# Optimization experiments

Measured on AMD Instinct MI355X. Metric: run time of the kernel, lower is better.

The kernel has to match this reference:

```python
import jax, jax.numpy as jnp
import numpy as np

N_AA = 300000
N_PROT = 30000
D_AA = 128
D_PROT = 128
HID = 128
OUT = 64
E_AP = 300000
E_PP = 960000
BATCH = 16384
NEG_SLOPE = 0.2


def _gatv2(x_src, x_dst, src, dst, Wl, bl, Wr, br, att, bias, num_dst):
    # GATv2Conv (heads=1): e_ij = att . leaky_relu(Wl x_j + Wr x_i); softmax over dst; out_i = sum alpha_ij * (Wl x_j) + bias
    xl = x_src @ Wl + bl                      # [Ns, C]
    xr = x_dst @ Wr + br                      # [Nd, C]
    e = jax.nn.leaky_relu(xl[src] + xr[dst], NEG_SLOPE)   # [E, C]
    logits = e @ att                          # [E]
    lmax = jax.ops.segment_max(logits, dst, num_segments=num_dst)
    ex = jnp.exp(logits - lmax[dst])
    denom = jax.ops.segment_sum(ex, dst, num_segments=num_dst)
    alpha = ex / denom[dst]                   # [E]
    msg = xl[src] * alpha[:, None]            # [E, C]
    out = jax.ops.segment_sum(msg, dst, num_segments=num_dst)
    return out + bias


def setup_inputs() -> dict:
    key = jax.random.key(0)
    ks = jax.random.split(key, 16)
    s = 0.05
    x_aa = jax.random.normal(ks[0], (N_AA, D_AA), jnp.float32)
    x_prot = jax.random.normal(ks[1], (N_PROT, D_PROT), jnp.float32)
    edge_index_ap = jnp.stack([
        jax.random.randint(ks[2], (E_AP,), 0, N_AA),
        jax.random.randint(ks[3], (E_AP,), 0, N_PROT)])
    edge_index_pp = jnp.stack([
        jax.random.randint(ks[4], (E_PP,), 0, N_PROT),
        jax.random.randint(ks[5], (E_PP,), 0, N_PROT)])
    return {
        'x_aa': x_aa, 'x_prot': x_prot,
        'edge_index_ap': edge_index_ap, 'edge_index_pp': edge_index_pp,
        'batch_size': BATCH,
        'Wl_ap': s * jax.random.normal(ks[6], (D_AA, HID), jnp.float32),
        'bl_ap': jnp.zeros((HID,), jnp.float32),
        'Wr_ap': s * jax.random.normal(ks[7], (D_PROT, HID), jnp.float32),
        'br_ap': jnp.zeros((HID,), jnp.float32),
        'att_ap': s * jax.random.normal(ks[8], (HID,), jnp.float32),
        'bias_ap': jnp.zeros((HID,), jnp.float32),
        'Wl_pp': s * jax.random.normal(ks[9], (D_PROT, HID), jnp.float32),
        'bl_pp': jnp.zeros((HID,), jnp.float32),
        'Wr_pp': s * jax.random.normal(ks[10], (D_PROT, HID), jnp.float32),
        'br_pp': jnp.zeros((HID,), jnp.float32),
        'att_pp': s * jax.random.normal(ks[11], (HID,), jnp.float32),
        'bias_pp': jnp.zeros((HID,), jnp.float32),
        'W_lin': s * jax.random.normal(ks[12], (HID, OUT), jnp.float32),
        'b_lin': jnp.zeros((OUT,), jnp.float32),
    }


def reference(x_aa, x_prot, edge_index_ap, edge_index_pp, batch_size,
              Wl_ap, bl_ap, Wr_ap, br_ap, att_ap, bias_ap,
              Wl_pp, bl_pp, Wr_pp, br_pp, att_pp, bias_pp,
              W_lin, b_lin):
    out_ap = _gatv2(x_aa, x_prot, edge_index_ap[0], edge_index_ap[1],
                    Wl_ap, bl_ap, Wr_ap, br_ap, att_ap, bias_ap, N_PROT)
    out_pp = _gatv2(x_prot, x_prot, edge_index_pp[0], edge_index_pp[1],
                    Wl_pp, bl_pp, Wr_pp, br_pp, att_pp, bias_pp, N_PROT)
    x = out_ap + out_pp                      # HeteroConv aggr='sum'
    x = jax.nn.relu(x[:batch_size])
    return x @ W_lin + b_lin
```

## Files before the change

kernel.cpp:

```cpp
#include <hip/hip_runtime.h>
#include <hip/hip_bf16.h>

typedef __attribute__((ext_vector_type(8))) short short8;
typedef __attribute__((ext_vector_type(4))) unsigned short ushort4_t;
typedef __attribute__((ext_vector_type(4))) float f32x4;

#define CAP_AP 64
#define CAP_PP 128

__device__ __forceinline__ unsigned short f2bf(float f) {
  unsigned u = __float_as_uint(f);
  u += 0x7FFFu + ((u >> 16) & 1u);
  return (unsigned short)(u >> 16);
}

__global__ __launch_bounds__(256) void k_init(
    int* __restrict__ map, int* __restrict__ cnt_ap, int* __restrict__ cnt_pp,
    int* __restrict__ ccount, int n_aa, int batch)
{
  int i = blockIdx.x * 256 + threadIdx.x;
  if (i < n_aa) map[i] = -1;
  if (i < batch) { cnt_ap[i] = 0; cnt_pp[i] = 0; }
  if (i == 0) *ccount = 0;
}

__global__ __launch_bounds__(256) void k_edges(
    const int* __restrict__ ei_ap, const int* __restrict__ ei_pp,
    int* __restrict__ map, int* __restrict__ cnt_ap, int* __restrict__ cnt_pp,
    int* __restrict__ csr_ap, int* __restrict__ csr_pp,
    int e_ap, int e_pp, int nb_ap, int batch)
{
  int b = blockIdx.x;
  if (b < nb_ap) {
    int e = b * 256 + threadIdx.x;
    if (e < e_ap) {
      int d = ei_ap[e_ap + e];
      if (d < batch) {
        int s = ei_ap[e];
        int pos = atomicAdd(&cnt_ap[d], 1);
        if (pos < CAP_AP) csr_ap[d * CAP_AP + pos] = s;
        map[s] = 1;
      }
    }
  } else {
    int e = (b - nb_ap) * 256 + threadIdx.x;
    if (e < e_pp) {
      int d = ei_pp[e_pp + e];
      if (d < batch) {
        int pos = atomicAdd(&cnt_pp[d], 1);
        if (pos < CAP_PP) csr_pp[d * CAP_PP + pos] = ei_pp[e];
      }
    }
  }
}

__global__ __launch_bounds__(256) void k_assign(
    int* __restrict__ map, int* __restrict__ inv, int* __restrict__ ccount, int n)
{
  int i = blockIdx.x * 256 + threadIdx.x;
  bool need = (i < n) && (map[i] == 1);
  unsigned long long m = __ballot(need);
  if (m == 0ull) return;
  int lane = threadIdx.x & 63;
  int pre = __popcll(m & ((1ull << lane) - 1ull));
  int leader = __ffsll((unsigned long long)m) - 1;
  int base = 0;
  if (lane == leader) base = atomicAdd(ccount, __popcll(m));
  base = __shfl(base, leader, 64);
  if (need) {
    int slot = base + pre;
    map[i] = slot;
    inv[slot] = i;
  }
}

struct GemmJob {
  const float* X; const int* inv; const int* rowsp; int M;
  const float* W; const float* bias; unsigned short* Y; int nb;
};

__device__ __forceinline__ void gemm_body(const GemmJob& J, int bid, short8* lwb)
{
  const int tid = threadIdx.x;
  const int rows = J.rowsp ? *J.rowsp : J.M;

  {
    unsigned short* lw16 = (unsigned short*)lwb;
#pragma unroll
    for (int p = 0; p < 16; ++p) {
      int fi = p * 1024 + tid * 4;
      float4 w4 = *(const float4*)(J.W + fi);
#pragma unroll
      for (int q = 0; q < 4; ++q) {
        int k = (fi + q) >> 7, n = (fi + q) & 127;
        float wv = (q == 0) ? w4.x : (q == 1) ? w4.y : (q == 2) ? w4.z : w4.w;
        lw16[(((k >> 5) * 8 + (n >> 4)) * 64 + ((k >> 3) & 3) * 16 + (n & 15)) * 8 + (k & 7)] = f2bf(wv);
      }
    }
  }

  const int wave = tid >> 6;
  const int lane = tid & 63;
  const int quad = lane >> 4;
  const int l16  = lane & 15;
  __syncthreads();

  for (int tile = bid; tile * 64 < rows; tile += J.nb) {
    int ra = tile * 64 + wave * 16 + l16;
    long xrow = -1;
    if (ra < rows) xrow = J.inv ? (long)J.inv[ra] : (long)ra;

    short8 xf[4];
#pragma unroll
    for (int kt = 0; kt < 4; ++kt) {
      short8 a = {};
      if (xrow >= 0) {
        const float* p = J.X + xrow * 128 + kt * 32 + quad * 8;
        float4 x0 = ((const float4*)p)[0];
        float4 x1 = ((const float4*)p)[1];
        a[0] = (short)f2bf(x0.x); a[1] = (short)f2bf(x0.y);
        a[2] = (short)f2bf(x0.z); a[3] = (short)f2bf(x0.w);
        a[4] = (short)f2bf(x1.x); a[5] = (short)f2bf(x1.y);
        a[6] = (short)f2bf(x1.z); a[7] = (short)f2bf(x1.w);
      }
      xf[kt] = a;
    }

    f32x4 accs[8];
#pragma unroll
    for (int nt = 0; nt < 8; ++nt) {
      f32x4 acc = {0.f, 0.f, 0.f, 0.f};
#pragma unroll
      for (int kt = 0; kt < 4; ++kt)
        acc = __builtin_amdgcn_mfma_f32_16x16x32_bf16(lwb[(kt * 8 + nt) * 64 + lane], xf[kt], acc, 0, 0, 0);
      accs[nt] = acc;
    }

    if (ra < rows) {
      unsigned short* yp = J.Y + (long)ra * 128;
#pragma unroll
      for (int nt = 0; nt < 8; ++nt) {
        int col = nt * 16 + quad * 4;
        float4 bv = *(const float4*)(J.bias + col);
        ushort4_t v;
        v[0] = f2bf(accs[nt][0] + bv.x);
        v[1] = f2bf(accs[nt][1] + bv.y);
        v[2] = f2bf(accs[nt][2] + bv.z);
        v[3] = f2bf(accs[nt][3] + bv.w);
        *(ushort4_t*)(yp + col) = v;
      }
    }
  }
}

__global__ __launch_bounds__(256) void k_mega(
    GemmJob j0, GemmJob j1, GemmJob j2, GemmJob j3,
    const int* __restrict__ map, const int* __restrict__ cnt_ap,
    int* __restrict__ csr_ap, int nb_gemm, int nb_remap, int batch)
{
  __shared__ short8 lwb[4 * 8 * 64];
  int b = blockIdx.x;
  if (b < nb_gemm) {
    if (b < j0.nb)                      gemm_body(j0, b, lwb);
    else if (b < j0.nb + j1.nb)         gemm_body(j1, b - j0.nb, lwb);
    else if (b < j0.nb + j1.nb + j2.nb) gemm_body(j2, b - j0.nb - j1.nb, lwb);
    else                                gemm_body(j3, b - j0.nb - j1.nb - j2.nb, lwb);
  } else {
    int i = (b - nb_gemm) * 256 + threadIdx.x;
    if (i < batch * CAP_AP) {
      int d = i / CAP_AP;
      int slot = i - d * CAP_AP;
      int n = cnt_ap[d]; if (n > CAP_AP) n = CAP_AP;
      if (slot < n) csr_ap[i] = map[csr_ap[i]];
    }
  }
}

__global__ __launch_bounds__(256) void k_gat_final(
    const int* __restrict__ cnt_ap, const int* __restrict__ csr_ap,
    const unsigned short* __restrict__ xl_aa,
    const unsigned short* __restrict__ xr_ap, const float* __restrict__ att_ap,
    const int* __restrict__ cnt_pp, const int* __restrict__ csr_pp,
    const unsigned short* __restrict__ xl_pp,
    const unsigned short* __restrict__ xr_pp, const float* __restrict__ att_pp,
    const float* __restrict__ bias_ap, const float* __restrict__ bias_pp,
    const float* __restrict__ W_lin, const float* __restrict__ b_lin,
    float* __restrict__ out, int batch)
{
  __shared__ unsigned lw2[64 * 64];
  __shared__ float lh[4][128];
  for (int e = threadIdx.x; e < 4096; e += 256) {
    int cp = e >> 6, o = e & 63;
    unsigned lo = f2bf(W_lin[(2 * cp) * 64 + o]);
    unsigned hi = f2bf(W_lin[(2 * cp + 1) * 64 + o]);
    lw2[e] = lo | (hi << 16);
  }

  const int wave = threadIdx.x >> 6;
  const int lane = threadIdx.x & 63;
  const int dst = blockIdx.x * 4 + wave;
  const int c0 = 2 * lane;

  float h0 = 0.f, h1 = 0.f;
  if (dst < batch) {
    h0 = bias_ap[c0] + bias_pp[c0];
    h1 = bias_ap[c0 + 1] + bias_pp[c0 + 1];

#pragma unroll
    for (int type = 0; type < 2; ++type) {
      const int* cnt  = type ? cnt_pp : cnt_ap;
      const int* csr  = type ? csr_pp : csr_ap;
      const int cap   = type ? CAP_PP : CAP_AP;
      const unsigned short* xl = type ? xl_pp : xl_aa;
      const unsigned short* xr = type ? xr_pp : xr_ap;
      const float* att = type ? att_pp : att_ap;

      int n = __builtin_amdgcn_readfirstlane(cnt[dst]);
      if (n > cap) n = cap;
      const long base = (long)dst * cap;
      unsigned upr = *(const unsigned*)(xr + (long)dst * 128 + c0);
      float xr0 = __uint_as_float(upr << 16);
      float xr1 = __uint_as_float(upr & 0xffff0000u);
      float2 at = *(const float2*)(att + c0);

      float l = 0.f, o0 = 0.f, o1 = 0.f;
      int j = 0;
      for (; j + 4 <= n; j += 4) {
        int si[4]; unsigned u[4];
#pragma unroll
        for (int q = 0; q < 4; ++q) si[q] = csr[base + j + q];
#pragma unroll
        for (int q = 0; q < 4; ++q)
          u[q] = *(const unsigned*)(xl + (long)si[q] * 128 + c0);
        float pv[4], a0v[4], a1v[4];
#pragma unroll
        for (int q = 0; q < 4; ++q) {
          float a0 = __uint_as_float(u[q] << 16);
          float a1 = __uint_as_float(u[q] & 0xffff0000u);
          a0v[q] = a0; a1v[q] = a1;
          float e0 = a0 + xr0; e0 = e0 > 0.f ? e0 : 0.2f * e0;
          float e1 = a1 + xr1; e1 = e1 > 0.f ? e1 : 0.2f * e1;
          pv[q] = at.x * e0 + at.y * e1;
        }
#pragma unroll
        for (int off = 32; off; off >>= 1) {
#pragma unroll
          for (int q = 0; q < 4; ++q) pv[q] += __shfl_xor(pv[q], off, 64);
        }
#pragma unroll
        for (int q = 0; q < 4; ++q) {
          float w = __expf(pv[q]);
          l += w;
          o0 = fmaf(w, a0v[q], o0);
          o1 = fmaf(w, a1v[q], o1);
        }
      }
      for (; j < n; ++j) {
        int sA = csr[base + j];
        unsigned uA = *(const unsigned*)(xl + (long)sA * 128 + c0);
        float a0 = __uint_as_float(uA << 16), a1 = __uint_as_float(uA & 0xffff0000u);
        float e0 = a0 + xr0; e0 = e0 > 0.f ? e0 : 0.2f * e0;
        float e1 = a1 + xr1; e1 = e1 > 0.f ? e1 : 0.2f * e1;
        float pA = at.x * e0 + at.y * e1;
#pragma unroll
        for (int off = 32; off; off >>= 1) pA += __shfl_xor(pA, off, 64);
        float w = __expf(pA);
        l += w;
        o0 = fmaf(w, a0, o0);
        o1 = fmaf(w, a1, o1);
      }
      float invl = (l > 0.f) ? 1.f / l : 0.f;
      h0 = fmaf(o0, invl, h0);
      h1 = fmaf(o1, invl, h1);
    }
  }

  lh[wave][c0]     = h0 > 0.f ? h0 : 0.f;
  lh[wave][c0 + 1] = h1 > 0.f ? h1 : 0.f;
  __syncthreads();

  if (dst < batch) {
    float acc = b_lin[lane];
#pragma unroll 16
    for (int cp = 0; cp < 64; ++cp) {
      unsigned u = lw2[cp * 64 + lane];
      acc = fmaf(lh[wave][2 * cp],     __uint_as_float(u << 16),        acc);
      acc = fmaf(lh[wave][2 * cp + 1], __uint_as_float(u & 0xffff0000u), acc);
    }
    out[(long)dst * 64 + lane] = acc;
  }
}

extern "C" void kernel_launch(void* const* d_in, const int* in_sizes, int n_in,
                              void* d_out, int out_size, void* d_ws, size_t ws_size,
                              hipStream_t stream)
{
  const float* x_aa   = (const float*)d_in[0];
  const float* x_prot = (const float*)d_in[1];
  const int*   ei_ap  = (const int*)d_in[2];
  const int*   ei_pp  = (const int*)d_in[3];
  const float* Wl_ap  = (const float*)d_in[5];
  const float* bl_ap  = (const float*)d_in[6];
  const float* Wr_ap  = (const float*)d_in[7];
  const float* br_ap  = (const float*)d_in[8];
  const float* att_ap = (const float*)d_in[9];
  const float* bias_ap= (const float*)d_in[10];
  const float* Wl_pp  = (const float*)d_in[11];
  const float* bl_pp  = (const float*)d_in[12];
  const float* Wr_pp  = (const float*)d_in[13];
  const float* br_pp  = (const float*)d_in[14];
  const float* att_pp = (const float*)d_in[15];
  const float* bias_pp= (const float*)d_in[16];
  const float* W_lin  = (const float*)d_in[17];
  const float* b_lin  = (const float*)d_in[18];
  float* out = (float*)d_out;

  const int D = 128;
  const int n_aa   = in_sizes[0] / D;
  const int n_prot = in_sizes[1] / D;
  const int e_ap   = in_sizes[2] / 2;
  const int e_pp   = in_sizes[3] / 2;
  const int batch  = out_size / 64;

  char* p = (char*)d_ws;
  auto take = [&](size_t n) { char* r = p; p += (n + 255) & ~(size_t)255; return r; };
  unsigned short* xlc_aa = (unsigned short*)take((size_t)n_aa * D * 2);
  unsigned short* xl_pp  = (unsigned short*)take((size_t)n_prot * D * 2);
  unsigned short* xr_ap  = (unsigned short*)take((size_t)batch * D * 2);
  unsigned short* xr_pp  = (unsigned short*)take((size_t)batch * D * 2);
  int* map      = (int*)take((size_t)n_aa * 4);
  int* inv      = (int*)take((size_t)n_aa * 4);
  int* ccount   = (int*)take(4);
  int* cnt_ap   = (int*)take((size_t)batch * 4);
  int* cnt_pp   = (int*)take((size_t)batch * 4);
  int* csr_ap   = (int*)take((size_t)batch * CAP_AP * 4);
  int* csr_pp   = (int*)take((size_t)batch * CAP_PP * 4);
  (void)ws_size; (void)n_in;

  const int nb_ap = (e_ap + 255) / 256;
  const int nb_pp = (e_pp + 255) / 256;
  const int nb_init = (n_aa + 255) / 256;

  k_init<<<nb_init, 256, 0, stream>>>(map, cnt_ap, cnt_pp, ccount, n_aa, batch);
  k_edges<<<nb_ap + nb_pp, 256, 0, stream>>>(
      ei_ap, ei_pp, map, cnt_ap, cnt_pp, csr_ap, csr_pp,
      e_ap, e_pp, nb_ap, batch);
  k_assign<<<nb_init, 256, 0, stream>>>(map, inv, ccount, n_aa);

  GemmJob j0{x_aa,   inv,     ccount,  0,      Wl_ap, bl_ap, xlc_aa, 1024};
  GemmJob j1{x_prot, nullptr, nullptr, n_prot, Wl_pp, bl_pp, xl_pp,  (n_prot + 63) / 64};
  GemmJob j2{x_prot, nullptr, nullptr, batch,  Wr_ap, br_ap, xr_ap,  (batch + 63) / 64};
  GemmJob j3{x_prot, nullptr, nullptr, batch,  Wr_pp, br_pp, xr_pp,  (batch + 63) / 64};
  const int nb_gemm = j0.nb + j1.nb + j2.nb + j3.nb;
  const int nb_remap = (batch * CAP_AP + 255) / 256;
  k_mega<<<nb_gemm + nb_remap, 256, 0, stream>>>(
      j0, j1, j2, j3, map, cnt_ap, csr_ap, nb_gemm, nb_remap, batch);

  k_gat_final<<<(batch + 3) / 4, 256, 0, stream>>>(
      cnt_ap, csr_ap, xlc_aa, xr_ap, att_ap,
      cnt_pp, csr_pp, xl_pp, xr_pp, att_pp,
      bias_ap, bias_pp, W_lin, b_lin, out, batch);
}
```

Before: 477.6 us.

## Process four edges per wave with 16-lane groups and 16-byte gathers

```diff
diff --git a/kernel.cpp b/kernel.cpp
--- a/kernel.cpp
+++ b/kernel.cpp
@@ -57,18 +57,26 @@
 __global__ __launch_bounds__(256) void k_assign(
     int* __restrict__ map, int* __restrict__ inv, int* __restrict__ ccount, int n)
 {
+  __shared__ int wb[4];
   int i = blockIdx.x * 256 + threadIdx.x;
   bool need = (i < n) && (map[i] == 1);
   unsigned long long m = __ballot(need);
-  if (m == 0ull) return;
+  int wave = threadIdx.x >> 6;
   int lane = threadIdx.x & 63;
-  int pre = __popcll(m & ((1ull << lane) - 1ull));
-  int leader = __ffsll((unsigned long long)m) - 1;
-  int base = 0;
-  if (lane == leader) base = atomicAdd(ccount, __popcll(m));
-  base = __shfl(base, leader, 64);
+  if (lane == 0) wb[wave] = __popcll(m);
+  __syncthreads();
+  if (threadIdx.x == 0) {
+    int t0 = wb[0], t1 = wb[1], t2 = wb[2], t3 = wb[3];
+    int tot = t0 + t1 + t2 + t3;
+    int base = tot ? atomicAdd(ccount, tot) : 0;
+    wb[0] = base;
+    wb[1] = base + t0;
+    wb[2] = base + t0 + t1;
+    wb[3] = base + t0 + t1 + t2;
+  }
+  __syncthreads();
   if (need) {
-    int slot = base + pre;
+    int slot = wb[wave] + __popcll(m & ((1ull << lane) - 1ull));
     map[i] = slot;
     inv[slot] = i;
   }
@@ -198,13 +206,23 @@
 
   const int wave = threadIdx.x >> 6;
   const int lane = threadIdx.x & 63;
-  const int dst = blockIdx.x * 4 + wave;
-  const int c0 = 2 * lane;
-
-  float h0 = 0.f, h1 = 0.f;
+  const int g    = lane >> 4;
+  const int l16  = lane & 15;
+  const int cb   = l16 * 8;
+  const int dst  = blockIdx.x * 4 + wave;
+
+  float h[8];
   if (dst < batch) {
-    h0 = bias_ap[c0] + bias_pp[c0];
-    h1 = bias_ap[c0 + 1] + bias_pp[c0 + 1];
+    {
+      float4 ba0 = *(const float4*)(bias_ap + cb);
+      float4 ba1 = *(const float4*)(bias_ap + cb + 4);
+      float4 bp0 = *(const float4*)(bias_pp + cb);
+      float4 bp1 = *(const float4*)(bias_pp + cb + 4);
+      h[0] = ba0.x + bp0.x; h[1] = ba0.y + bp0.y;
+      h[2] = ba0.z + bp0.z; h[3] = ba0.w + bp0.w;
+      h[4] = ba1.x + bp1.x; h[5] = ba1.y + bp1.y;
+      h[6] = ba1.z + bp1.z; h[7] = ba1.w + bp1.w;
+    }
 
 #pragma unroll
     for (int type = 0; type < 2; ++type) {
@@ -218,65 +236,82 @@
       int n = __builtin_amdgcn_readfirstlane(cnt[dst]);
       if (n > cap) n = cap;
       const long base = (long)dst * cap;
-      unsigned upr = *(const unsigned*)(xr + (long)dst * 128 + c0);
-      float xr0 = __uint_as_float(upr << 16);
-      float xr1 = __uint_as_float(upr & 0xffff0000u);
-      float2 at = *(const float2*)(att + c0);
-
-      float l = 0.f, o0 = 0.f, o1 = 0.f;
-      int j = 0;
-      for (; j + 4 <= n; j += 4) {
-        int si[4]; unsigned u[4];
-#pragma unroll
-        for (int q = 0; q < 4; ++q) si[q] = csr[base + j + q];
-#pragma unroll
-        for (int q = 0; q < 4; ++q)
-          u[q] = *(const unsigned*)(xl + (long)si[q] * 128 + c0);
-        float pv[4], a0v[4], a1v[4];
-#pragma unroll
-        for (int q = 0; q < 4; ++q) {
-          float a0 = __uint_as_float(u[q] << 16);
-          float a1 = __uint_as_float(u[q] & 0xffff0000u);
-          a0v[q] = a0; a1v[q] = a1;
-          float e0 = a0 + xr0; e0 = e0 > 0.f ? e0 : 0.2f * e0;
-          float e1 = a1 + xr1; e1 = e1 > 0.f ? e1 : 0.2f * e1;
-          pv[q] = at.x * e0 + at.y * e1;
+
+      float xrv[8], atv[8];
+      {
+        short8 uxr = *(const short8*)(xr + (long)dst * 128 + cb);
+#pragma unroll
+        for (int k = 0; k < 8; ++k)
+          xrv[k] = __uint_as_float(((unsigned)(unsigned short)uxr[k]) << 16);
+        float4 a0 = *(const float4*)(att + cb);
+        float4 a1 = *(const float4*)(att + cb + 4);
+        atv[0] = a0.x; atv[1] = a0.y; atv[2] = a0.z; atv[3] = a0.w;
+        atv[4] = a1.x; atv[5] = a1.y; atv[6] = a1.z; atv[7] = a1.w;
+      }
+
+      float l = 0.f, o[8];
+#pragma unroll
+      for (int k = 0; k < 8; ++k) o[k] = 0.f;
+
+      if (n > 0) {
+        bool act = g < n;
+        int si = act ? csr[base + g] : 0;
+        short8 ua = *(const short8*)(xl + (long)si * 128 + cb);
+        int niter = (n + 3) >> 2;
+        for (int it = 0; it < niter; ++it) {
+          int en = it * 4 + 4 + g;
+          bool actn = en < n;
+          int sin = actn ? csr[base + en] : 0;
+          short8 uan = *(const short8*)(xl + (long)sin * 128 + cb);
+
+          float a[8];
+#pragma unroll
+          for (int k = 0; k < 8; ++k)
+            a[k] = __uint_as_float(((unsigned)(unsigned short)ua[k]) << 16);
+          float p = 0.f;
+#pragma unroll
+          for (int k = 0; k < 8; ++k) {
+            float e = a[k] + xrv[k];
+            e = e > 0.f ? e : 0.2f * e;
+            p = fmaf(atv[k], e, p);
+          }
+          p += __shfl_xor(p, 8, 64);
+          p += __shfl_xor(p, 4, 64);
+          p += __shfl_xor(p, 2, 64);
+          p += __shfl_xor(p, 1, 64);
+          float w = act ? __expf(p) : 0.f;
+          l += w;
+#pragma unroll
+          for (int k = 0; k < 8; ++k) o[k] = fmaf(w, a[k], o[k]);
+
+          ua = uan; act = actn;
         }
-#pragma unroll
-        for (int off = 32; off; off >>= 1) {
-#pragma unroll
-          for (int q = 0; q < 4; ++q) pv[q] += __shfl_xor(pv[q], off, 64);
-        }
-#pragma unroll
-        for (int q = 0; q < 4; ++q) {
-          float w = __expf(pv[q]);
-          l += w;
-          o0 = fmaf(w, a0v[q], o0);
-          o1 = fmaf(w, a1v[q], o1);
-        }
-      }
-      for (; j < n; ++j) {
-        int sA = csr[base + j];
-        unsigned uA = *(const unsigned*)(xl + (long)sA * 128 + c0);
-        float a0 = __uint_as_float(uA << 16), a1 = __uint_as_float(uA & 0xffff0000u);
-        float e0 = a0 + xr0; e0 = e0 > 0.f ? e0 : 0.2f * e0;
-        float e1 = a1 + xr1; e1 = e1 > 0.f ? e1 : 0.2f * e1;
-        float pA = at.x * e0 + at.y * e1;
-#pragma unroll
-        for (int off = 32; off; off >>= 1) pA += __shfl_xor(pA, off, 64);
-        float w = __expf(pA);
-        l += w;
-        o0 = fmaf(w, a0, o0);
-        o1 = fmaf(w, a1, o1);
+      }
+      l += __shfl_xor(l, 16, 64);
+      l += __shfl_xor(l, 32, 64);
+#pragma unroll
+      for (int k = 0; k < 8; ++k) {
+        o[k] += __shfl_xor(o[k], 16, 64);
+        o[k] += __shfl_xor(o[k], 32, 64);
       }
       float invl = (l > 0.f) ? 1.f / l : 0.f;
-      h0 = fmaf(o0, invl, h0);
-      h1 = fmaf(o1, invl, h1);
-    }
-  }
-
-  lh[wave][c0]     = h0 > 0.f ? h0 : 0.f;
-  lh[wave][c0 + 1] = h1 > 0.f ? h1 : 0.f;
+#pragma unroll
+      for (int k = 0; k < 8; ++k) h[k] = fmaf(o[k], invl, h[k]);
+    }
+  } else {
+#pragma unroll
+    for (int k = 0; k < 8; ++k) h[k] = 0.f;
+  }
+
+  if (g == 0) {
+    float4 r0, r1;
+    r0.x = h[0] > 0.f ? h[0] : 0.f; r0.y = h[1] > 0.f ? h[1] : 0.f;
+    r0.z = h[2] > 0.f ? h[2] : 0.f; r0.w = h[3] > 0.f ? h[3] : 0.f;
+    r1.x = h[4] > 0.f ? h[4] : 0.f; r1.y = h[5] > 0.f ? h[5] : 0.f;
+    r1.z = h[6] > 0.f ? h[6] : 0.f; r1.w = h[7] > 0.f ? h[7] : 0.f;
+    *(float4*)&lh[wave][cb]     = r0;
+    *(float4*)&lh[wave][cb + 4] = r1;
+  }
   __syncthreads();
 
   if (dst < batch) {
```

Measured after the change: 426.9 us. 10.6% less time.
